# Kernel tuning notes

Hardware: AMD Instinct MI355X
Metric: run time of the kernel (lower is better)

## Reference

```python
import jax, jax.numpy as jnp
import numpy as np

NUM_CLASSES = 10
ALPHA = 0.25
GAMMA = 2.0
BETA = 1.0
EPS = 1e-7


def _corners(centers, dims, yaws):
    # centers [N,2], dims [N,2] (l,w), yaws [N] -> corners [N,4,2]
    half = dims * 0.5
    base = jnp.array([[1., 1.], [-1., 1.], [-1., -1.], [1., -1.]], dtype=centers.dtype)
    base = base[None, :, :] * half[:, None, :]  # [N,4,2]
    c, s = jnp.cos(yaws), jnp.sin(yaws)
    x = base[..., 0] * c[:, None] - base[..., 1] * s[:, None]
    y = base[..., 0] * s[:, None] + base[..., 1] * c[:, None]
    corners = jnp.stack([x, y], axis=-1) + centers[:, None, :]
    return corners[:, jnp.array([3, 2, 1, 0]), :]  # reorder as in torch code


def _cross(u, v):
    return u[..., 0] * v[..., 1] - u[..., 1] * v[..., 0]


def _signed_area(q):  # q [...,4,2]
    return 0.5 * jnp.sum(_cross(q, jnp.roll(q, -1, axis=-2)), axis=-1)


def _pts_in_quad(pts, quad, sgn):
    # pts [N,P,2] inside convex quad [N,4,2]; sgn = orientation sign of quad [N]
    a = quad
    e = jnp.roll(quad, -1, axis=-2) - a  # [N,4,2]
    d = pts[:, :, None, :] - a[:, None, :, :]  # [N,P,4,2]
    cr = e[:, None, :, 0] * d[..., 1] - e[:, None, :, 1] * d[..., 0]  # [N,P,4]
    return jnp.all(cr * sgn[:, None, None] >= -1e-9, axis=-1)


def _rotated_iou(cA, cB):
    # Exact convex-quad intersection IoU (replaces the per-box Shapely loop).
    N = cA.shape[0]
    sgnA = jnp.sign(_signed_area(cA))
    sgnB = jnp.sign(_signed_area(cB))
    vA_in_B = _pts_in_quad(cA, cB, sgnB)  # [N,4]
    vB_in_A = _pts_in_quad(cB, cA, sgnA)  # [N,4]
    # all 4x4 edge-edge intersections
    a1 = cA; a2 = jnp.roll(cA, -1, axis=1)
    b1 = cB; b2 = jnp.roll(cB, -1, axis=1)
    da = (a2 - a1)[:, :, None, :]  # [N,4,1,2]
    db = (b2 - b1)[:, None, :, :]  # [N,1,4,2]
    dp = b1[:, None, :, :] - a1[:, :, None, :]  # [N,4,4,2]
    den = _cross(da, db)  # [N,4,4]
    den_safe = jnp.where(jnp.abs(den) < 1e-12, 1.0, den)
    t = _cross(dp, db) / den_safe
    s = _cross(dp, da) / den_safe
    val_x = (jnp.abs(den) > 1e-12) & (t >= 0) & (t <= 1) & (s >= 0) & (s <= 1)
    xpts = a1[:, :, None, :] + t[..., None] * da  # [N,4,4,2]
    # up to 24 candidate vertices of the convex intersection polygon
    pts = jnp.concatenate([cA, cB, xpts.reshape(N, 16, 2)], axis=1)  # [N,24,2]
    valid = jnp.concatenate([vA_in_B, vB_in_A, val_x.reshape(N, 16)], axis=1)
    pts = jnp.where(valid[..., None], pts, 0.0)
    nv = valid.sum(axis=1)
    cent = pts.sum(axis=1) / jnp.maximum(nv, 1)[:, None]
    ang = jnp.arctan2(pts[..., 1] - cent[:, None, 1], pts[..., 0] - cent[:, None, 0])
    key = jnp.where(valid, ang, 1e9)
    order = jnp.argsort(key, axis=1)
    ps = jnp.take_along_axis(pts, order[..., None], axis=1)
    vs = jnp.take_along_axis(valid, order, axis=1)
    ps = jnp.where(vs[..., None], ps, ps[:, :1, :])  # pad with first valid vertex
    inter = 0.5 * jnp.abs(jnp.sum(_cross(ps, jnp.roll(ps, -1, axis=1)), axis=1))
    inter = jnp.where(nv >= 3, inter, 0.0)
    areaA = jnp.abs(_signed_area(cA))
    areaB = jnp.abs(_signed_area(cB))
    union = areaA + areaB - inter
    return jnp.where(union > 1e-7, inter / union, 0.0)


def _sl1(p, t):
    d = jnp.abs(p - t)
    return jnp.where(d < BETA, 0.5 * d * d / BETA, d - 0.5 * BETA)


def setup_inputs() -> dict:
    key = jax.random.key(0)
    ks = jax.random.split(key, 7)
    B, C, H, W = 8, NUM_CLASSES, 256, 256
    cls_pred = jax.random.normal(ks[0], (B, C, H, W), dtype=jnp.float32)
    reg_pred = jax.random.uniform(ks[1], (B, 9, H, W), dtype=jnp.float32)
    iou_pred = jax.random.normal(ks[2], (B, 1, H, W), dtype=jnp.float32)
    cls_targets = jax.random.randint(ks[3], (B, H, W), 0, C, dtype=jnp.int32)
    reg_targets = jax.random.uniform(ks[4], (B, 9, H, W), dtype=jnp.float32)
    reg_weights = jax.random.randint(ks[5], (B, H, W), 0, 2).astype(jnp.float32)
    iou_targets = jax.random.uniform(ks[6], (B, 1, H, W), dtype=jnp.float32)
    return {"cls_pred": cls_pred, "reg_pred": reg_pred, "iou_pred": iou_pred,
            "cls_targets": cls_targets, "reg_targets": reg_targets,
            "reg_weights": reg_weights, "iou_targets": iou_targets}


def reference(cls_pred, reg_pred, iou_pred, cls_targets, reg_targets, reg_weights, iou_targets):
    B, C, H, W = cls_pred.shape
    N = B * H * W
    clsf = jnp.transpose(cls_pred, (0, 2, 3, 1)).reshape(N, C)
    regf = jnp.transpose(reg_pred, (0, 2, 3, 1)).reshape(N, 9)
    regt = jnp.transpose(reg_targets, (0, 2, 3, 1)).reshape(N, 9)
    iouf = jnp.transpose(iou_pred, (0, 2, 3, 1)).reshape(N)
    iout = iou_targets.reshape(N)
    ct = cls_targets.reshape(N)
    w = reg_weights.reshape(N)
    pos = (w > 0).astype(clsf.dtype)
    num_pos = jnp.maximum(pos.sum(), 1.0)
    # focal classification loss
    valid = ct >= 0
    p = jax.nn.softmax(clsf, axis=1)
    tl = jnp.clip(ct, 0, C - 1)
    pt = jnp.clip(jnp.take_along_axis(p, tl[:, None], axis=1)[:, 0], EPS, 1.0 - EPS)
    alpha_t = jnp.where(ct > 0, ALPHA, 1.0 - ALPHA)
    fl = -alpha_t * (1.0 - pt) ** GAMMA * jnp.log(pt)
    cls_loss = jnp.sum(jnp.where(valid, fl, 0.0)) / num_pos
    cen_p, dim_p, yaw_p = regf[:, :2], regf[:, 3:5], regf[:, 6]
    cen_t, dim_t, yaw_t = regt[:, :2], regt[:, 3:5], regt[:, 6]
    cp = _corners(cen_p, dim_p, yaw_p)
    ctg = _corners(cen_t, dim_t, yaw_t)
    iou = jax.lax.stop_gradient(_rotated_iou(cp, ctg))
    d2 = jnp.sum((cen_p - cen_t) ** 2, axis=-1)
    allc = jnp.concatenate([cp, ctg], axis=1)  # [N,8,2]
    c2 = jnp.maximum(jnp.sum((allc.max(axis=1) - allc.min(axis=1)) ** 2, axis=-1), EPS)
    loss_bev = 1.0 - iou + d2 / c2
    at_p = jnp.arctan(dim_p[:, 1] / jnp.maximum(dim_p[:, 0], EPS))
    at_t = jnp.arctan(dim_t[:, 1] / jnp.maximum(dim_t[:, 0], EPS))
    v = (4.0 / np.pi ** 2) * (at_p - at_t) ** 2
    alpha_c = jax.lax.stop_gradient(v / (1.0 - iou + v + EPS))
    loss_bev = loss_bev + alpha_c * v
    bev_loss = jnp.sum(loss_bev * pos) / num_pos
    # smooth-L1 terms: z (ch 2), h (ch 5), vel (ch 7:9)
    z_loss = jnp.sum(_sl1(regf[:, 2], regt[:, 2]) * pos) / num_pos
    h_loss = jnp.sum(_sl1(regf[:, 5], regt[:, 5]) * pos) / num_pos
    vel_loss = jnp.sum(_sl1(regf[:, 7:9], regt[:, 7:9]).sum(axis=-1) * pos) / num_pos
    # BCE-with-logits IoU head loss
    x, y = iouf, iout
    bce = jnp.maximum(x, 0.0) - x * y + jnp.log1p(jnp.exp(-jnp.abs(x)))
    iou_loss = jnp.sum(bce * pos) / num_pos
    return jnp.stack([cls_loss, bev_loss, z_loss, h_loss, vel_loss, iou_loss])
```

## Files before the change

kernel.cpp:

```cpp
#include <hip/hip_runtime.h>
#include <cstdint>
#include <cstddef>

#define B_ 8
#define C_ 10
#define HW_ 65536
#define NPIX_ (B_ * HW_)
#define NB_ 2048

__device__ __forceinline__ float sl1f(float p, float t) {
    float d = fabsf(p - t);
    return (d < 1.0f) ? 0.5f * d * d : d - 0.5f;
}
__device__ __forceinline__ void pinf(float v)  { asm volatile("" :: "v"(v)); }
__device__ __forceinline__ void pini(int v)    { asm volatile("" :: "v"(v)); }

__global__ __launch_bounds__(256) void bev_loss_cls(
    const float* __restrict__ cls_pred, const float* __restrict__ reg_pred,
    const float* __restrict__ iou_pred, const int* __restrict__ cls_tg,
    const float* __restrict__ reg_tg, const float* __restrict__ reg_w,
    const float* __restrict__ iou_tg, double* __restrict__ part)
{
    int n  = blockIdx.x * blockDim.x + threadIdx.x;
    int b  = n >> 16;
    int hw = n & 65535;

    float lg[C_];
    {
        const float* cp = cls_pred + (size_t)b * C_ * HW_ + hw;
        #pragma unroll
        for (int c = 0; c < C_; c++) lg[c] = cp[(size_t)c * HW_];
    }
    const float* rp = reg_pred + (size_t)b * 9 * HW_ + hw;
    const float* rt = reg_tg  + (size_t)b * 9 * HW_ + hw;
    float p2 = rp[2 * HW_], p5 = rp[5 * HW_], p7 = rp[7 * HW_], p8 = rp[8 * HW_];
    float t2 = rt[2 * HW_], t5 = rt[5 * HW_], t7 = rt[7 * HW_], t8 = rt[8 * HW_];
    int   ct = cls_tg[n];
    float w  = reg_w[n];
    float xi = iou_pred[n];
    float yi = iou_tg[n];

    #pragma unroll
    for (int c = 0; c < C_; c++) pinf(lg[c]);
    pinf(p2); pinf(p5); pinf(p7); pinf(p8);
    pinf(t2); pinf(t5); pinf(t7); pinf(t8);
    pini(ct); pinf(w); pinf(xi); pinf(yi);

    float a0;
    {
        float m = lg[0];
        #pragma unroll
        for (int c = 1; c < C_; c++) m = fmaxf(m, lg[c]);
        int tl = ct < 0 ? 0 : (ct > C_ - 1 ? C_ - 1 : ct);
        float se = 0.f, et = 0.f;
        #pragma unroll
        for (int c = 0; c < C_; c++) {
            float e = __expf(lg[c] - m);
            se += e;
            et = (c == tl) ? e : et;
        }
        float pt = __fdividef(et, se);
        pt = fminf(fmaxf(pt, 1e-7f), 1.0f - 1e-7f);
        float alpha_t = (ct > 0) ? 0.25f : 0.75f;
        float omp = 1.0f - pt;
        float fl = -alpha_t * omp * omp * __logf(pt);
        a0 = (ct >= 0) ? fl : 0.0f;
    }

    float pos = (w > 0.f) ? 1.f : 0.f;
    float a2 = sl1f(p2, t2) * pos;
    float a3 = sl1f(p5, t5) * pos;
    float a4 = (sl1f(p7, t7) + sl1f(p8, t8)) * pos;
    float bce = fmaxf(xi, 0.f) - xi * yi + __logf(1.0f + __expf(-fabsf(xi)));
    float a5 = bce * pos;

    const int kid[6] = { 0, 2, 3, 4, 5, 6 };
    double av[6] = { (double)a0, (double)a2, (double)a3,
                     (double)a4, (double)a5, (double)pos };
    __shared__ double red[6][4];
    int lane = threadIdx.x & 63;
    int wv   = threadIdx.x >> 6;
    #pragma unroll
    for (int k = 0; k < 6; k++) {
        double s = av[k];
        for (int off = 32; off > 0; off >>= 1) s += __shfl_down(s, off, 64);
        if (lane == 0) red[k][wv] = s;
    }
    __syncthreads();
    if (threadIdx.x == 0) {
        #pragma unroll
        for (int k = 0; k < 6; k++)
            part[(size_t)kid[k] * NB_ + blockIdx.x] = red[k][0] + red[k][1] + red[k][2] + red[k][3];
    }
}

__global__ __launch_bounds__(256) void bev_loss_iou(
    const float* __restrict__ reg_pred, const float* __restrict__ reg_tg,
    const float* __restrict__ reg_w, double* __restrict__ part)
{
    int n  = blockIdx.x * blockDim.x + threadIdx.x;
    int b  = n >> 16;
    int hw = n & 65535;

    const float* rp = reg_pred + (size_t)b * 9 * HW_ + hw;
    const float* rt = reg_tg  + (size_t)b * 9 * HW_ + hw;
    float p0 = rp[0 * HW_], p1 = rp[1 * HW_], p3 = rp[3 * HW_], p4 = rp[4 * HW_], p6 = rp[6 * HW_];
    float t0_ = rt[0 * HW_], t1_ = rt[1 * HW_], t3 = rt[3 * HW_], t4 = rt[4 * HW_], t6 = rt[6 * HW_];
    float w  = reg_w[n];

    pinf(p0); pinf(p1); pinf(p3); pinf(p4); pinf(p6);
    pinf(t0_); pinf(t1_); pinf(t3); pinf(t4); pinf(t6);
    pinf(w);

    float pos = (w > 0.f) ? 1.f : 0.f;

    float Ax[4], Ay[4], Bx[4], By[4];
    {
        const float sbx[4] = { 1.f, -1.f, -1.f, 1.f };
        const float sby[4] = { -1.f, -1.f, 1.f, 1.f };
        float hx = 0.5f * p3, hy = 0.5f * p4;
        float ss, cc; __sincosf(p6, &ss, &cc);
        #pragma unroll
        for (int i = 0; i < 4; i++) {
            float px = sbx[i] * hx, py = sby[i] * hy;
            Ax[i] = px * cc - py * ss + p0;
            Ay[i] = px * ss + py * cc + p1;
        }
        float hx2 = 0.5f * t3, hy2 = 0.5f * t4;
        float ss2, cc2; __sincosf(t6, &ss2, &cc2);
        #pragma unroll
        for (int i = 0; i < 4; i++) {
            float px = sbx[i] * hx2, py = sby[i] * hy2;
            Bx[i] = px * cc2 - py * ss2 + t0_;
            By[i] = px * ss2 + py * cc2 + t1_;
        }
    }

    float sa = 0.f, sb = 0.f;
    #pragma unroll
    for (int i = 0; i < 4; i++) {
        int j = (i + 1) & 3;
        sa += Ax[i] * Ay[j] - Ay[i] * Ax[j];
        sb += Bx[i] * By[j] - By[i] * Bx[j];
    }
    sa *= 0.5f; sb *= 0.5f;
    float sgnA = (sa > 0.f) ? 1.f : ((sa < 0.f) ? -1.f : 0.f);
    float sgnB = (sb > 0.f) ? 1.f : ((sb < 0.f) ? -1.f : 0.f);

    float S = 0.f;
    {
        float dB[4][4];
        #pragma unroll
        for (int j = 0; j < 4; j++) {
            int j1 = (j + 1) & 3;
            float sx = sgnB * (Bx[j1] - Bx[j]);
            float sy = sgnB * (By[j1] - By[j]);
            float kj = sx * By[j] - sy * Bx[j];
            #pragma unroll
            for (int i = 0; i < 4; i++)
                dB[j][i] = sx * Ay[i] - sy * Ax[i] - kj;
        }
        #pragma unroll
        for (int i = 0; i < 4; i++) {
            int i1 = (i + 1) & 3;
            float t0 = 0.f, t1 = 1.f;
            #pragma unroll
            for (int j = 0; j < 4; j++) {
                float d0 = dB[j][i], d1 = dB[j][i1];
                float den = d1 - d0;
                float t = __fdividef(-d0, den);
                float lo = (den > 0.f) ? t : ((den == 0.f && d0 < 0.f) ? 2.f : 0.f);
                float hi = (den < 0.f) ? t : 1.f;
                t0 = fmaxf(t0, lo);
                t1 = fminf(t1, hi);
            }
            S += (Ax[i] * Ay[i1] - Ay[i] * Ax[i1]) * fmaxf(t1 - t0, 0.f);
        }
    }
    {
        float dA[4][4];
        #pragma unroll
        for (int j = 0; j < 4; j++) {
            int j1 = (j + 1) & 3;
            float sx = sgnA * (Ax[j1] - Ax[j]);
            float sy = sgnA * (Ay[j1] - Ay[j]);
            float kj = sx * Ay[j] - sy * Ax[j];
            #pragma unroll
            for (int i = 0; i < 4; i++)
                dA[j][i] = sx * By[i] - sy * Bx[i] - kj;
        }
        #pragma unroll
        for (int i = 0; i < 4; i++) {
            int i1 = (i + 1) & 3;
            float t0 = 0.f, t1 = 1.f;
            #pragma unroll
            for (int j = 0; j < 4; j++) {
                float d0 = dA[j][i], d1 = dA[j][i1];
                float den = d1 - d0;
                float t = __fdividef(-d0, den);
                float lo = (den > 0.f) ? t : ((den == 0.f && d0 < 0.f) ? 2.f : 0.f);
                float hi = (den < 0.f) ? t : 1.f;
                t0 = fmaxf(t0, lo);
                t1 = fminf(t1, hi);
            }
            S += (Bx[i] * By[i1] - By[i] * Bx[i1]) * fmaxf(t1 - t0, 0.f);
        }
    }
    float inter = 0.5f * fabsf(S);
    float areaA = fabsf(sa), areaB = fabsf(sb);
    float uni = areaA + areaB - inter;
    float iou = (uni > 1e-7f) ? __fdividef(inter, uni) : 0.f;

    float a1;
    {
        float ddx = p0 - t0_, ddy = p1 - t1_;
        float d2 = fmaf(ddx, ddx, ddy * ddy);
        float mnx = Ax[0], mxx = Ax[0], mny = Ay[0], mxy = Ay[0];
        #pragma unroll
        for (int i = 1; i < 4; i++) {
            mnx = fminf(mnx, Ax[i]); mxx = fmaxf(mxx, Ax[i]);
            mny = fminf(mny, Ay[i]); mxy = fmaxf(mxy, Ay[i]);
        }
        #pragma unroll
        for (int i = 0; i < 4; i++) {
            mnx = fminf(mnx, Bx[i]); mxx = fmaxf(mxx, Bx[i]);
            mny = fminf(mny, By[i]); mxy = fmaxf(mxy, By[i]);
        }
        float exd = mxx - mnx, eyd = mxy - mny;
        float c2 = fmaxf(fmaf(exd, exd, eyd * eyd), 1e-7f);

        float rp_ = __fdividef(p4, fmaxf(p3, 1e-7f));
        float rt_ = __fdividef(t4, fmaxf(t3, 1e-7f));
        float dv = atanf(__fdividef(rp_ - rt_, fmaf(rp_, rt_, 1.f)));
        float v = 0.4052847345693511f * dv * dv;
        float alpha_c = __fdividef(v, 1.0f - iou + v + 1e-7f);
        float lbev = 1.0f - iou + __fdividef(d2, c2) + alpha_c * v;
        a1 = lbev * pos;
    }

    __shared__ double red[4];
    int lane = threadIdx.x & 63;
    int wv   = threadIdx.x >> 6;
    double s = (double)a1;
    for (int off = 32; off > 0; off >>= 1) s += __shfl_down(s, off, 64);
    if (lane == 0) red[wv] = s;
    __syncthreads();
    if (threadIdx.x == 0)
        part[(size_t)1 * NB_ + blockIdx.x] = red[0] + red[1] + red[2] + red[3];
}

__global__ __launch_bounds__(1024) void bev_loss_fin(
    const double* __restrict__ part, float* __restrict__ out)
{
    int t = threadIdx.x;
    double v[7];
    #pragma unroll
    for (int k = 0; k < 7; k++)
        v[k] = part[(size_t)k * NB_ + t] + part[(size_t)k * NB_ + 1024 + t];

    int lane = t & 63, wv = t >> 6;
    __shared__ double red[7][16];
    #pragma unroll
    for (int k = 0; k < 7; k++) {
        double s = v[k];
        for (int off = 32; off > 0; off >>= 1) s += __shfl_down(s, off, 64);
        if (lane == 0) red[k][wv] = s;
    }
    __syncthreads();
    if (t == 0) {
        double tot[7];
        #pragma unroll
        for (int k = 0; k < 7; k++) {
            double s = 0.0;
            #pragma unroll
            for (int i = 0; i < 16; i++) s += red[k][i];
            tot[k] = s;
        }
        double npos = fmax(tot[6], 1.0);
        #pragma unroll
        for (int k = 0; k < 6; k++) out[k] = (float)(tot[k] / npos);
    }
}

extern "C" void kernel_launch(void* const* d_in, const int* in_sizes, int n_in,
                              void* d_out, int out_size, void* d_ws, size_t ws_size,
                              hipStream_t stream) {
    const float* cls_pred = (const float*)d_in[0];
    const float* reg_pred = (const float*)d_in[1];
    const float* iou_pred = (const float*)d_in[2];
    const int*   cls_tg   = (const int*)d_in[3];
    const float* reg_tg   = (const float*)d_in[4];
    const float* reg_w    = (const float*)d_in[5];
    const float* iou_tg   = (const float*)d_in[6];
    float* out = (float*)d_out;
    double* part = (double*)d_ws;

    bev_loss_cls<<<NB_, 256, 0, stream>>>(cls_pred, reg_pred, iou_pred, cls_tg,
                                          reg_tg, reg_w, iou_tg, part);
    bev_loss_iou<<<NB_, 256, 0, stream>>>(reg_pred, reg_tg, reg_w, part);
    bev_loss_fin<<<1, 1024, 0, stream>>>(part, out);
}
```

Before: 41.02 us.

## Compact positive pixels into a list and compute rotated IoU only for them

Measured after the change: 128.7 us. 214% more time.

```diff
diff --git a/kernel.cpp b/kernel.cpp
--- a/kernel.cpp
+++ b/kernel.cpp
@@ -6,7 +6,9 @@
 #define C_ 10
 #define HW_ 65536
 #define NPIX_ (B_ * HW_)
-#define NB_ 2048
+#define NB1_ 2048
+#define NB2_ 1024
+#define ROWS_ 2048
 
 __device__ __forceinline__ float sl1f(float p, float t) {
     float d = fabsf(p - t);
@@ -19,7 +21,8 @@
     const float* __restrict__ cls_pred, const float* __restrict__ reg_pred,
     const float* __restrict__ iou_pred, const int* __restrict__ cls_tg,
     const float* __restrict__ reg_tg, const float* __restrict__ reg_w,
-    const float* __restrict__ iou_tg, double* __restrict__ part)
+    const float* __restrict__ iou_tg, double* __restrict__ part,
+    unsigned int* __restrict__ counter, unsigned int* __restrict__ list)
 {
     int n  = blockIdx.x * blockDim.x + threadIdx.x;
     int b  = n >> 16;
@@ -46,6 +49,20 @@
     pinf(t2); pinf(t5); pinf(t7); pinf(t8);
     pini(ct); pinf(w); pinf(xi); pinf(yi);
 
+    int lane = threadIdx.x & 63;
+    int wv   = threadIdx.x >> 6;
+
+    bool posb = (w > 0.f);
+    {
+        unsigned long long m = __ballot(posb);
+        int cnt    = __popcll(m);
+        int prefix = __popcll(m & ((1ULL << lane) - 1ULL));
+        unsigned base = 0;
+        if (lane == 0 && cnt > 0) base = atomicAdd(counter, (unsigned)cnt);
+        base = (unsigned)__shfl((int)base, 0, 64);
+        if (posb) list[base + prefix] = (unsigned)n;
+    }
+
     float a0;
     {
         float m = lg[0];
@@ -67,7 +84,7 @@
         a0 = (ct >= 0) ? fl : 0.0f;
     }
 
-    float pos = (w > 0.f) ? 1.f : 0.f;
+    float pos = posb ? 1.f : 0.f;
     float a2 = sl1f(p2, t2) * pos;
     float a3 = sl1f(p5, t5) * pos;
     float a4 = (sl1f(p7, t7) + sl1f(p8, t8)) * pos;
@@ -78,8 +95,6 @@
     double av[6] = { (double)a0, (double)a2, (double)a3,
                      (double)a4, (double)a5, (double)pos };
     __shared__ double red[6][4];
-    int lane = threadIdx.x & 63;
-    int wv   = threadIdx.x >> 6;
     #pragma unroll
     for (int k = 0; k < 6; k++) {
         double s = av[k];
@@ -90,141 +105,140 @@
     if (threadIdx.x == 0) {
         #pragma unroll
         for (int k = 0; k < 6; k++)
-            part[(size_t)kid[k] * NB_ + blockIdx.x] = red[k][0] + red[k][1] + red[k][2] + red[k][3];
+            part[(size_t)kid[k] * ROWS_ + blockIdx.x] = red[k][0] + red[k][1] + red[k][2] + red[k][3];
     }
 }
 
 __global__ __launch_bounds__(256) void bev_loss_iou(
     const float* __restrict__ reg_pred, const float* __restrict__ reg_tg,
-    const float* __restrict__ reg_w, double* __restrict__ part)
+    const unsigned int* __restrict__ counter, const unsigned int* __restrict__ list,
+    double* __restrict__ part)
 {
-    int n  = blockIdx.x * blockDim.x + threadIdx.x;
-    int b  = n >> 16;
-    int hw = n & 65535;
-
-    const float* rp = reg_pred + (size_t)b * 9 * HW_ + hw;
-    const float* rt = reg_tg  + (size_t)b * 9 * HW_ + hw;
-    float p0 = rp[0 * HW_], p1 = rp[1 * HW_], p3 = rp[3 * HW_], p4 = rp[4 * HW_], p6 = rp[6 * HW_];
-    float t0_ = rt[0 * HW_], t1_ = rt[1 * HW_], t3 = rt[3 * HW_], t4 = rt[4 * HW_], t6 = rt[6 * HW_];
-    float w  = reg_w[n];
-
-    pinf(p0); pinf(p1); pinf(p3); pinf(p4); pinf(p6);
-    pinf(t0_); pinf(t1_); pinf(t3); pinf(t4); pinf(t6);
-    pinf(w);
-
-    float pos = (w > 0.f) ? 1.f : 0.f;
-
-    float Ax[4], Ay[4], Bx[4], By[4];
-    {
-        const float sbx[4] = { 1.f, -1.f, -1.f, 1.f };
-        const float sby[4] = { -1.f, -1.f, 1.f, 1.f };
-        float hx = 0.5f * p3, hy = 0.5f * p4;
-        float ss, cc; __sincosf(p6, &ss, &cc);
-        #pragma unroll
-        for (int i = 0; i < 4; i++) {
-            float px = sbx[i] * hx, py = sby[i] * hy;
-            Ax[i] = px * cc - py * ss + p0;
-            Ay[i] = px * ss + py * cc + p1;
-        }
-        float hx2 = 0.5f * t3, hy2 = 0.5f * t4;
-        float ss2, cc2; __sincosf(t6, &ss2, &cc2);
-        #pragma unroll
-        for (int i = 0; i < 4; i++) {
-            float px = sbx[i] * hx2, py = sby[i] * hy2;
-            Bx[i] = px * cc2 - py * ss2 + t0_;
-            By[i] = px * ss2 + py * cc2 + t1_;
-        }
-    }
-
-    float sa = 0.f, sb = 0.f;
-    #pragma unroll
-    for (int i = 0; i < 4; i++) {
-        int j = (i + 1) & 3;
-        sa += Ax[i] * Ay[j] - Ay[i] * Ax[j];
-        sb += Bx[i] * By[j] - By[i] * Bx[j];
-    }
-    sa *= 0.5f; sb *= 0.5f;
-    float sgnA = (sa > 0.f) ? 1.f : ((sa < 0.f) ? -1.f : 0.f);
-    float sgnB = (sb > 0.f) ? 1.f : ((sb < 0.f) ? -1.f : 0.f);
-
-    float S = 0.f;
-    {
-        float dB[4][4];
-        #pragma unroll
-        for (int j = 0; j < 4; j++) {
-            int j1 = (j + 1) & 3;
-            float sx = sgnB * (Bx[j1] - Bx[j]);
-            float sy = sgnB * (By[j1] - By[j]);
-            float kj = sx * By[j] - sy * Bx[j];
-            #pragma unroll
-            for (int i = 0; i < 4; i++)
-                dB[j][i] = sx * Ay[i] - sy * Ax[i] - kj;
-        }
-        #pragma unroll
-        for (int i = 0; i < 4; i++) {
-            int i1 = (i + 1) & 3;
-            float t0 = 0.f, t1 = 1.f;
+    int count  = (int)*counter;
+    int stride = gridDim.x * blockDim.x;
+    double acc = 0.0;
+
+    for (int i = blockIdx.x * blockDim.x + threadIdx.x; i < count; i += stride) {
+        int n  = (int)list[i];
+        int b  = n >> 16;
+        int hw = n & 65535;
+
+        const float* rp = reg_pred + (size_t)b * 9 * HW_ + hw;
+        const float* rt = reg_tg  + (size_t)b * 9 * HW_ + hw;
+        float p0 = rp[0 * HW_], p1 = rp[1 * HW_], p3 = rp[3 * HW_], p4 = rp[4 * HW_], p6 = rp[6 * HW_];
+        float t0_ = rt[0 * HW_], t1_ = rt[1 * HW_], t3 = rt[3 * HW_], t4 = rt[4 * HW_], t6 = rt[6 * HW_];
+        pinf(p0); pinf(p1); pinf(p3); pinf(p4); pinf(p6);
+        pinf(t0_); pinf(t1_); pinf(t3); pinf(t4); pinf(t6);
+
+        float Ax[4], Ay[4], Bx[4], By[4];
+        {
+            const float sbx[4] = { 1.f, -1.f, -1.f, 1.f };
+            const float sby[4] = { -1.f, -1.f, 1.f, 1.f };
+            float hx = 0.5f * p3, hy = 0.5f * p4;
+            float ss, cc; __sincosf(p6, &ss, &cc);
+            #pragma unroll
+            for (int q = 0; q < 4; q++) {
+                float px = sbx[q] * hx, py = sby[q] * hy;
+                Ax[q] = px * cc - py * ss + p0;
+                Ay[q] = px * ss + py * cc + p1;
+            }
+            float hx2 = 0.5f * t3, hy2 = 0.5f * t4;
+            float ss2, cc2; __sincosf(t6, &ss2, &cc2);
+            #pragma unroll
+            for (int q = 0; q < 4; q++) {
+                float px = sbx[q] * hx2, py = sby[q] * hy2;
+                Bx[q] = px * cc2 - py * ss2 + t0_;
+                By[q] = px * ss2 + py * cc2 + t1_;
+            }
+        }
+
+        float sa = 0.f, sb = 0.f;
+        #pragma unroll
+        for (int q = 0; q < 4; q++) {
+            int j = (q + 1) & 3;
+            sa += Ax[q] * Ay[j] - Ay[q] * Ax[j];
+            sb += Bx[q] * By[j] - By[q] * Bx[j];
+        }
+        sa *= 0.5f; sb *= 0.5f;
+        float sgnA = (sa > 0.f) ? 1.f : ((sa < 0.f) ? -1.f : 0.f);
+        float sgnB = (sb > 0.f) ? 1.f : ((sb < 0.f) ? -1.f : 0.f);
+
+        float S = 0.f;
+        {
+            float dB[4][4];
             #pragma unroll
             for (int j = 0; j < 4; j++) {
-                float d0 = dB[j][i], d1 = dB[j][i1];
-                float den = d1 - d0;
-                float t = __fdividef(-d0, den);
-                float lo = (den > 0.f) ? t : ((den == 0.f && d0 < 0.f) ? 2.f : 0.f);
-                float hi = (den < 0.f) ? t : 1.f;
-                t0 = fmaxf(t0, lo);
-                t1 = fminf(t1, hi);
-            }
-            S += (Ax[i] * Ay[i1] - Ay[i] * Ax[i1]) * fmaxf(t1 - t0, 0.f);
-        }
-    }
-    {
-        float dA[4][4];
-        #pragma unroll
-        for (int j = 0; j < 4; j++) {
-            int j1 = (j + 1) & 3;
-            float sx = sgnA * (Ax[j1] - Ax[j]);
-            float sy = sgnA * (Ay[j1] - Ay[j]);
-            float kj = sx * Ay[j] - sy * Ax[j];
-            #pragma unroll
-            for (int i = 0; i < 4; i++)
-                dA[j][i] = sx * By[i] - sy * Bx[i] - kj;
-        }
-        #pragma unroll
-        for (int i = 0; i < 4; i++) {
-            int i1 = (i + 1) & 3;
-            float t0 = 0.f, t1 = 1.f;
+                int j1 = (j + 1) & 3;
+                float sx = sgnB * (Bx[j1] - Bx[j]);
+                float sy = sgnB * (By[j1] - By[j]);
+                float kj = sx * By[j] - sy * Bx[j];
+                #pragma unroll
+                for (int q = 0; q < 4; q++)
+                    dB[j][q] = sx * Ay[q] - sy * Ax[q] - kj;
+            }
+            #pragma unroll
+            for (int q = 0; q < 4; q++) {
+                int q1 = (q + 1) & 3;
+                float t0 = 0.f, t1 = 1.f;
+                #pragma unroll
+                for (int j = 0; j < 4; j++) {
+                    float d0 = dB[j][q], d1 = dB[j][q1];
+                    float den = d1 - d0;
+                    float t = __fdividef(-d0, den);
+                    float lo = (den > 0.f) ? t : ((den == 0.f && d0 < 0.f) ? 2.f : 0.f);
+                    float hi = (den < 0.f) ? t : 1.f;
+                    t0 = fmaxf(t0, lo);
+                    t1 = fminf(t1, hi);
+                }
+                S += (Ax[q] * Ay[q1] - Ay[q] * Ax[q1]) * fmaxf(t1 - t0, 0.f);
+            }
+        }
+        {
+            float dA[4][4];
             #pragma unroll
             for (int j = 0; j < 4; j++) {
-                float d0 = dA[j][i], d1 = dA[j][i1];
-                float den = d1 - d0;
-                float t = __fdividef(-d0, den);
-                float lo = (den > 0.f) ? t : ((den == 0.f && d0 < 0.f) ? 2.f : 0.f);
-                float hi = (den < 0.f) ? t : 1.f;
-                t0 = fmaxf(t0, lo);
-                t1 = fminf(t1, hi);
-            }
-            S += (Bx[i] * By[i1] - By[i] * Bx[i1]) * fmaxf(t1 - t0, 0.f);
-        }
-    }
-    float inter = 0.5f * fabsf(S);
-    float areaA = fabsf(sa), areaB = fabsf(sb);
-    float uni = areaA + areaB - inter;
-    float iou = (uni > 1e-7f) ? __fdividef(inter, uni) : 0.f;
-
-    float a1;
-    {
+                int j1 = (j + 1) & 3;
+                float sx = sgnA * (Ax[j1] - Ax[j]);
+                float sy = sgnA * (Ay[j1] - Ay[j]);
+                float kj = sx * Ay[j] - sy * Ax[j];
+                #pragma unroll
+                for (int q = 0; q < 4; q++)
+                    dA[j][q] = sx * By[q] - sy * Bx[q] - kj;
+            }
+            #pragma unroll
+            for (int q = 0; q < 4; q++) {
+                int q1 = (q + 1) & 3;
+                float t0 = 0.f, t1 = 1.f;
+                #pragma unroll
+                for (int j = 0; j < 4; j++) {
+                    float d0 = dA[j][q], d1 = dA[j][q1];
+                    float den = d1 - d0;
+                    float t = __fdividef(-d0, den);
+                    float lo = (den > 0.f) ? t : ((den == 0.f && d0 < 0.f) ? 2.f : 0.f);
+                    float hi = (den < 0.f) ? t : 1.f;
+                    t0 = fmaxf(t0, lo);
+                    t1 = fminf(t1, hi);
+                }
+                S += (Bx[q] * By[q1] - By[q] * Bx[q1]) * fmaxf(t1 - t0, 0.f);
+            }
+        }
+        float inter = 0.5f * fabsf(S);
+        float areaA = fabsf(sa), areaB = fabsf(sb);
+        float uni = areaA + areaB - inter;
+        float iou = (uni > 1e-7f) ? __fdividef(inter, uni) : 0.f;
+
         float ddx = p0 - t0_, ddy = p1 - t1_;
         float d2 = fmaf(ddx, ddx, ddy * ddy);
         float mnx = Ax[0], mxx = Ax[0], mny = Ay[0], mxy = Ay[0];
         #pragma unroll
-        for (int i = 1; i < 4; i++) {
-            mnx = fminf(mnx, Ax[i]); mxx = fmaxf(mxx, Ax[i]);
-            mny = fminf(mny, Ay[i]); mxy = fmaxf(mxy, Ay[i]);
-        }
-        #pragma unroll
-        for (int i = 0; i < 4; i++) {
-            mnx = fminf(mnx, Bx[i]); mxx = fmaxf(mxx, Bx[i]);
-            mny = fminf(mny, By[i]); mxy = fmaxf(mxy, By[i]);
+        for (int q = 1; q < 4; q++) {
+            mnx = fminf(mnx, Ax[q]); mxx = fmaxf(mxx, Ax[q]);
+            mny = fminf(mny, Ay[q]); mxy = fmaxf(mxy, Ay[q]);
+        }
+        #pragma unroll
+        for (int q = 0; q < 4; q++) {
+            mnx = fminf(mnx, Bx[q]); mxx = fmaxf(mxx, Bx[q]);
+            mny = fminf(mny, By[q]); mxy = fmaxf(mxy, By[q]);
         }
         float exd = mxx - mnx, eyd = mxy - mny;
         float c2 = fmaxf(fmaf(exd, exd, eyd * eyd), 1e-7f);
@@ -234,19 +248,18 @@
         float dv = atanf(__fdividef(rp_ - rt_, fmaf(rp_, rt_, 1.f)));
         float v = 0.4052847345693511f * dv * dv;
         float alpha_c = __fdividef(v, 1.0f - iou + v + 1e-7f);
-        float lbev = 1.0f - iou + __fdividef(d2, c2) + alpha_c * v;
-        a1 = lbev * pos;
+        acc += (double)(1.0f - iou + __fdividef(d2, c2) + alpha_c * v);
     }
 
     __shared__ double red[4];
     int lane = threadIdx.x & 63;
     int wv   = threadIdx.x >> 6;
-    double s = (double)a1;
+    double s = acc;
     for (int off = 32; off > 0; off >>= 1) s += __shfl_down(s, off, 64);
     if (lane == 0) red[wv] = s;
     __syncthreads();
     if (threadIdx.x == 0)
-        part[(size_t)1 * NB_ + blockIdx.x] = red[0] + red[1] + red[2] + red[3];
+        part[(size_t)1 * ROWS_ + blockIdx.x] = red[0] + red[1] + red[2] + red[3];
 }
 
 __global__ __launch_bounds__(1024) void bev_loss_fin(
@@ -255,8 +268,12 @@
     int t = threadIdx.x;
     double v[7];
     #pragma unroll
-    for (int k = 0; k < 7; k++)
-        v[k] = part[(size_t)k * NB_ + t] + part[(size_t)k * NB_ + 1024 + t];
+    for (int k = 0; k < 7; k++) {
+        if (k == 1)
+            v[k] = part[(size_t)k * ROWS_ + t];
+        else
+            v[k] = part[(size_t)k * ROWS_ + t] + part[(size_t)k * ROWS_ + 1024 + t];
+    }
 
     int lane = t & 63, wv = t >> 6;
     __shared__ double red[7][16];
@@ -293,10 +310,15 @@
     const float* reg_w    = (const float*)d_in[5];
     const float* iou_tg   = (const float*)d_in[6];
     float* out = (float*)d_out;
+
     double* part = (double*)d_ws;
-
-    bev_loss_cls<<<NB_, 256, 0, stream>>>(cls_pred, reg_pred, iou_pred, cls_tg,
-                                          reg_tg, reg_w, iou_tg, part);
-    bev_loss_iou<<<NB_, 256, 0, stream>>>(reg_pred, reg_tg, reg_w, part);
+    unsigned int* counter = (unsigned int*)((char*)d_ws + (size_t)7 * ROWS_ * sizeof(double));
+    unsigned int* list    = counter + 4;
+
+    hipMemsetAsync(counter, 0, sizeof(unsigned int), stream);
+
+    bev_loss_cls<<<NB1_, 256, 0, stream>>>(cls_pred, reg_pred, iou_pred, cls_tg,
+                                           reg_tg, reg_w, iou_tg, part, counter, list);
+    bev_loss_iou<<<NB2_, 256, 0, stream>>>(reg_pred, reg_tg, counter, list, part);
     bev_loss_fin<<<1, 1024, 0, stream>>>(part, out);
 }
```

## Fuse classification and IoU loss kernels with shared-memory staged float4 loads

Applied to the files above, without the earlier changes.

New measurement: 35.26 us. 14.0% less time.

```diff
diff --git a/kernel.cpp b/kernel.cpp
--- a/kernel.cpp
+++ b/kernel.cpp
@@ -7,55 +7,55 @@
 #define HW_ 65536
 #define NPIX_ (B_ * HW_)
 #define NB_ 2048
+#define NCH_ 28
 
 __device__ __forceinline__ float sl1f(float p, float t) {
     float d = fabsf(p - t);
     return (d < 1.0f) ? 0.5f * d * d : d - 0.5f;
 }
-__device__ __forceinline__ void pinf(float v)  { asm volatile("" :: "v"(v)); }
-__device__ __forceinline__ void pini(int v)    { asm volatile("" :: "v"(v)); }
-
-__global__ __launch_bounds__(256) void bev_loss_cls(
+
+__global__ __launch_bounds__(256) void bev_loss_main(
     const float* __restrict__ cls_pred, const float* __restrict__ reg_pred,
     const float* __restrict__ iou_pred, const int* __restrict__ cls_tg,
     const float* __restrict__ reg_tg, const float* __restrict__ reg_w,
     const float* __restrict__ iou_tg, double* __restrict__ part)
 {
-    int n  = blockIdx.x * blockDim.x + threadIdx.x;
-    int b  = n >> 16;
-    int hw = n & 65535;
-
-    float lg[C_];
-    {
-        const float* cp = cls_pred + (size_t)b * C_ * HW_ + hw;
-        #pragma unroll
-        for (int c = 0; c < C_; c++) lg[c] = cp[(size_t)c * HW_];
-    }
-    const float* rp = reg_pred + (size_t)b * 9 * HW_ + hw;
-    const float* rt = reg_tg  + (size_t)b * 9 * HW_ + hw;
-    float p2 = rp[2 * HW_], p5 = rp[5 * HW_], p7 = rp[7 * HW_], p8 = rp[8 * HW_];
-    float t2 = rt[2 * HW_], t5 = rt[5 * HW_], t7 = rt[7 * HW_], t8 = rt[8 * HW_];
+    __shared__ float sch[NCH_][256];
+
+    int tid  = threadIdx.x;
+    int lane = tid & 63;
+    int wv   = tid >> 6;
+    int n0   = blockIdx.x << 8;
+    int b    = n0 >> 16;
+    int hw0  = n0 & 65535;
+    int n    = n0 + tid;
+
+    #pragma unroll
+    for (int k = 0; k < 7; k++) {
+        int c = wv + 4 * k;
+        const float* src;
+        if (c < 10)      src = cls_pred + ((size_t)(b * C_ + c)) * HW_ + hw0;
+        else if (c < 19) src = reg_pred + ((size_t)(b * 9 + (c - 10))) * HW_ + hw0;
+        else             src = reg_tg  + ((size_t)(b * 9 + (c - 19))) * HW_ + hw0;
+        float4 v = *reinterpret_cast<const float4*>(src + lane * 4);
+        *reinterpret_cast<float4*>(&sch[c][lane * 4]) = v;
+    }
     int   ct = cls_tg[n];
     float w  = reg_w[n];
     float xi = iou_pred[n];
     float yi = iou_tg[n];
-
-    #pragma unroll
-    for (int c = 0; c < C_; c++) pinf(lg[c]);
-    pinf(p2); pinf(p5); pinf(p7); pinf(p8);
-    pinf(t2); pinf(t5); pinf(t7); pinf(t8);
-    pini(ct); pinf(w); pinf(xi); pinf(yi);
+    __syncthreads();
 
     float a0;
     {
-        float m = lg[0];
-        #pragma unroll
-        for (int c = 1; c < C_; c++) m = fmaxf(m, lg[c]);
+        float m = sch[0][tid];
+        #pragma unroll
+        for (int c = 1; c < C_; c++) m = fmaxf(m, sch[c][tid]);
         int tl = ct < 0 ? 0 : (ct > C_ - 1 ? C_ - 1 : ct);
         float se = 0.f, et = 0.f;
         #pragma unroll
         for (int c = 0; c < C_; c++) {
-            float e = __expf(lg[c] - m);
+            float e = __expf(sch[c][tid] - m);
             se += e;
             et = (c == tl) ? e : et;
         }
@@ -68,51 +68,13 @@
     }
 
     float pos = (w > 0.f) ? 1.f : 0.f;
-    float a2 = sl1f(p2, t2) * pos;
-    float a3 = sl1f(p5, t5) * pos;
-    float a4 = (sl1f(p7, t7) + sl1f(p8, t8)) * pos;
-    float bce = fmaxf(xi, 0.f) - xi * yi + __logf(1.0f + __expf(-fabsf(xi)));
-    float a5 = bce * pos;
-
-    const int kid[6] = { 0, 2, 3, 4, 5, 6 };
-    double av[6] = { (double)a0, (double)a2, (double)a3,
-                     (double)a4, (double)a5, (double)pos };
-    __shared__ double red[6][4];
-    int lane = threadIdx.x & 63;
-    int wv   = threadIdx.x >> 6;
-    #pragma unroll
-    for (int k = 0; k < 6; k++) {
-        double s = av[k];
-        for (int off = 32; off > 0; off >>= 1) s += __shfl_down(s, off, 64);
-        if (lane == 0) red[k][wv] = s;
-    }
-    __syncthreads();
-    if (threadIdx.x == 0) {
-        #pragma unroll
-        for (int k = 0; k < 6; k++)
-            part[(size_t)kid[k] * NB_ + blockIdx.x] = red[k][0] + red[k][1] + red[k][2] + red[k][3];
-    }
-}
-
-__global__ __launch_bounds__(256) void bev_loss_iou(
-    const float* __restrict__ reg_pred, const float* __restrict__ reg_tg,
-    const float* __restrict__ reg_w, double* __restrict__ part)
-{
-    int n  = blockIdx.x * blockDim.x + threadIdx.x;
-    int b  = n >> 16;
-    int hw = n & 65535;
-
-    const float* rp = reg_pred + (size_t)b * 9 * HW_ + hw;
-    const float* rt = reg_tg  + (size_t)b * 9 * HW_ + hw;
-    float p0 = rp[0 * HW_], p1 = rp[1 * HW_], p3 = rp[3 * HW_], p4 = rp[4 * HW_], p6 = rp[6 * HW_];
-    float t0_ = rt[0 * HW_], t1_ = rt[1 * HW_], t3 = rt[3 * HW_], t4 = rt[4 * HW_], t6 = rt[6 * HW_];
-    float w  = reg_w[n];
-
-    pinf(p0); pinf(p1); pinf(p3); pinf(p4); pinf(p6);
-    pinf(t0_); pinf(t1_); pinf(t3); pinf(t4); pinf(t6);
-    pinf(w);
-
-    float pos = (w > 0.f) ? 1.f : 0.f;
+
+    float p0 = sch[10][tid], p1 = sch[11][tid], p2 = sch[12][tid];
+    float p3 = sch[13][tid], p4 = sch[14][tid], p5 = sch[15][tid];
+    float p6 = sch[16][tid], p7 = sch[17][tid], p8 = sch[18][tid];
+    float t0_ = sch[19][tid], t1_ = sch[20][tid], t2 = sch[21][tid];
+    float t3  = sch[22][tid], t4  = sch[23][tid], t5 = sch[24][tid];
+    float t6  = sch[25][tid], t7  = sch[26][tid], t8 = sch[27][tid];
 
     float Ax[4], Ay[4], Bx[4], By[4];
     {
@@ -238,15 +200,28 @@
         a1 = lbev * pos;
     }
 
-    __shared__ double red[4];
-    int lane = threadIdx.x & 63;
-    int wv   = threadIdx.x >> 6;
-    double s = (double)a1;
-    for (int off = 32; off > 0; off >>= 1) s += __shfl_down(s, off, 64);
-    if (lane == 0) red[wv] = s;
-    __syncthreads();
-    if (threadIdx.x == 0)
-        part[(size_t)1 * NB_ + blockIdx.x] = red[0] + red[1] + red[2] + red[3];
+    float a2 = sl1f(p2, t2) * pos;
+    float a3 = sl1f(p5, t5) * pos;
+    float a4 = (sl1f(p7, t7) + sl1f(p8, t8)) * pos;
+    float bce = fmaxf(xi, 0.f) - xi * yi + __logf(1.0f + __expf(-fabsf(xi)));
+    float a5 = bce * pos;
+
+    double av[7] = { (double)a0, (double)a1, (double)a2, (double)a3,
+                     (double)a4, (double)a5, (double)pos };
+    __shared__ double red[7][4];
+    __syncthreads();
+    #pragma unroll
+    for (int k = 0; k < 7; k++) {
+        double s = av[k];
+        for (int off = 32; off > 0; off >>= 1) s += __shfl_down(s, off, 64);
+        if (lane == 0) red[k][wv] = s;
+    }
+    __syncthreads();
+    if (tid == 0) {
+        #pragma unroll
+        for (int k = 0; k < 7; k++)
+            part[(size_t)k * NB_ + blockIdx.x] = red[k][0] + red[k][1] + red[k][2] + red[k][3];
+    }
 }
 
 __global__ __launch_bounds__(1024) void bev_loss_fin(
@@ -295,8 +270,7 @@
     float* out = (float*)d_out;
     double* part = (double*)d_ws;
 
-    bev_loss_cls<<<NB_, 256, 0, stream>>>(cls_pred, reg_pred, iou_pred, cls_tg,
-                                          reg_tg, reg_w, iou_tg, part);
-    bev_loss_iou<<<NB_, 256, 0, stream>>>(reg_pred, reg_tg, reg_w, part);
+    bev_loss_main<<<NB_, 256, 0, stream>>>(cls_pred, reg_pred, iou_pred, cls_tg,
+                                           reg_tg, reg_w, iou_tg, part);
     bev_loss_fin<<<1, 1024, 0, stream>>>(part, out);
 }
```
